# Kernel tuning notes

Hardware: AMD Instinct MI355X
Metric: run time of the kernel (lower is better)

Reference implementation:

```python
import jax, jax.numpy as jnp
import numpy as np

B, T, H, K = 2048, 200, 256, 8


def setup_inputs() -> dict:
    key = jax.random.key(0)
    ks = jax.random.split(key, 8)
    s = 1.0 / np.sqrt(H)  # torch nn.Linear default init range
    vm = jax.random.uniform(ks[5], (B, T)) < 0.6
    vm = vm.at[:, :3].set(True)  # guarantee >=3 valid visits so history_mask is non-empty
    return {
        "current_state": jax.random.normal(ks[0], (B, H), jnp.float32),
        "state_sequence": jax.random.normal(ks[1], (B, T, H), jnp.float32),
        "visit_mask": vm,
        "Wq": jax.random.uniform(ks[2], (H, H), jnp.float32, -s, s),
        "bq": jnp.zeros((H,), jnp.float32),
        "Wk": jax.random.uniform(ks[3], (H, H), jnp.float32, -s, s),
        "bk": jnp.zeros((H,), jnp.float32),
        "Wv": jax.random.uniform(ks[4], (H, H), jnp.float32, -s, s),
        "bv": jnp.zeros((H,), jnp.float32),
    }


def reference(current_state, state_sequence, visit_mask, Wq, bq, Wk, bk, Wv, bv):
    mask = visit_mask.astype(bool)
    valid_counts = mask.sum(axis=1)  # (B,)
    t_idx = jnp.arange(T)[None, :]
    # attend only to visits strictly before the last valid one
    history_mask = mask & (t_idx < (valid_counts - 1)[:, None])

    q = current_state @ Wq + bq                      # (B,H)
    k = state_sequence @ Wk + bk                     # (B,T,H)
    v = jax.nn.relu(state_sequence @ Wv + bv)        # dropout is identity in eval

    scores = jnp.einsum('bth,bh->bt', k, q) / np.sqrt(H).astype(np.float32)
    scores = jnp.where(history_mask, scores, -1e9)
    attn = jax.nn.softmax(scores, axis=-1)
    attn = jnp.where(history_mask, attn, 0.0)
    norm = attn.sum(-1, keepdims=True)
    attn = attn / jnp.where(norm > 0, norm, 1.0)

    # vectorized per-row top-K sparsify + renormalize (replaces the python loop)
    masked = jnp.where(history_mask, attn, -1.0)
    vals, idx = jax.lax.top_k(masked, K)             # (B,K)
    keep_vals = jnp.maximum(vals, 0.0)               # invalid slots had -1 -> contribute 0
    sparse = jnp.zeros_like(attn).at[jnp.arange(B)[:, None], idx].set(keep_vals)
    eps = jnp.finfo(attn.dtype).eps
    attn = sparse / jnp.maximum(sparse.sum(-1, keepdims=True), eps)

    summary = jnp.einsum('bth,bt->bh', v, attn)
    has_history = history_mask.any(axis=1, keepdims=True)
    summary = jnp.where(has_history, summary, 0.0)

    # selected visit indices (top-K of final weights, -1 where outside history)
    _, midx = jax.lax.top_k(jnp.where(history_mask, attn, -1.0), K)
    sel_mask = jnp.take_along_axis(history_mask, midx, axis=1)
    selected = jnp.where(sel_mask, midx, -1).astype(jnp.int32)

    return summary, attn, selected
```

## Files before the change

### kernel.cpp

```cpp
#include <hip/hip_runtime.h>
#include <cstddef>

#define BB 2048
#define TT 200
#define HH 256
#define KK 8
#define XP 260

#define WS_M2T 0
#define WS_D   65536
#define WS_E   65792
#define WS_F   66048
#define WS_IDX 66112
#define WS_W   82496

__global__ __launch_bounds__(256) void prep_kernel(
    const float* __restrict__ Wq, const float* __restrict__ bq,
    const float* __restrict__ Wk, const float* __restrict__ bk,
    float* __restrict__ M2T, float* __restrict__ dvec,
    float* __restrict__ evec, float* __restrict__ fsc) {
  const int l = blockIdx.x, i = threadIdx.x;
  __shared__ float s_wq[HH], s_bq[HH], s_bk[HH], s_red[HH];
  s_wq[i] = Wq[(size_t)l * HH + i];
  s_bq[i] = bq[i];
  s_bk[i] = bk[i];
  __syncthreads();
  const float* wk = Wk + (size_t)i * HH;
  float acc = 0.f, dd = 0.f;
#pragma unroll 8
  for (int j = 0; j < HH; ++j) {
    float wkj = wk[j];
    acc += s_wq[j] * wkj;
    dd  += s_bq[j] * wkj;
  }
  M2T[(size_t)l * HH + i] = acc;
  if (l == 0) dvec[i] = dd;
  s_red[i] = s_wq[i] * s_bk[i];
  __syncthreads();
  for (int s = 128; s > 0; s >>= 1) {
    if (i < s) s_red[i] += s_red[i + s];
    __syncthreads();
  }
  if (i == 0) {
    evec[l] = s_red[0];
    if (l == 0) {
      float ff = 0.f;
      for (int j = 0; j < HH; ++j) ff += s_bq[j] * s_bk[j];
      *fsc = ff;
    }
  }
}

__global__ __launch_bounds__(256) void attn_kernel(
    const float* __restrict__ CS, const float* __restrict__ X,
    const int* __restrict__ VM,
    const float* __restrict__ M2T, const float* __restrict__ dvec,
    const float* __restrict__ evec, const float* __restrict__ fsc,
    float* __restrict__ out, int* __restrict__ wsIdx, float* __restrict__ wsW) {
  const int tid = threadIdx.x, b = blockIdx.x;
  __shared__ float s_qk[HH], s_sc[TT], s_cand[TT], s_red[HH];
  __shared__ int   s_hist[TT];
  __shared__ int   s_cnt;
  __shared__ float s_qb, s_dS;
  __shared__ int   s_selI[KK];
  __shared__ float s_selV[KK];

  int m = 0;
  if (tid < TT) m = (VM[(size_t)b * TT + tid] != 0) ? 1 : 0;
  if (tid == 0) s_cnt = 0;
  __syncthreads();
  unsigned long long bal = __ballot(m);
  if ((tid & 63) == 0) atomicAdd(&s_cnt, (int)__popcll(bal));

  const float* csr = CS + (size_t)b * HH;
  float acc = dvec[tid];
#pragma unroll 4
  for (int l = 0; l < HH; ++l) acc += csr[l] * M2T[(size_t)l * HH + tid];
  s_qk[tid] = acc * 0.0625f;
  s_red[tid] = evec[tid] * csr[tid];
  __syncthreads();
  const int cnt = s_cnt;
  if (tid < TT) s_hist[tid] = (m && (tid < cnt - 1)) ? 1 : 0;
  for (int s = 128; s > 0; s >>= 1) {
    if (tid < s) s_red[tid] += s_red[tid + s];
    __syncthreads();
  }
  if (tid == 0) s_qb = (s_red[0] + fsc[0]) * 0.0625f;
  __syncthreads();

  {
    const int w = tid >> 6, lane = tid & 63;
    const float* xrow = X + (size_t)b * TT * HH;
    const float4 q4 = ((const float4*)s_qk)[lane];
    const float qb = s_qb;
#pragma unroll 2
    for (int t = w * 50; t < w * 50 + 50; ++t) {
      float4 xv = *(const float4*)(xrow + (size_t)t * HH + lane * 4);
      float p = xv.x * q4.x + xv.y * q4.y + xv.z * q4.z + xv.w * q4.w;
#pragma unroll
      for (int off = 32; off; off >>= 1) p += __shfl_xor(p, off);
      if (lane == 0) s_sc[t] = p + qb;
    }
  }
  __syncthreads();

  float v = (tid < TT && s_hist[tid]) ? s_sc[tid] : -3.4e38f;
  s_red[tid] = v;
  __syncthreads();
  for (int s = 128; s > 0; s >>= 1) {
    if (tid < s) s_red[tid] = fmaxf(s_red[tid], s_red[tid + s]);
    __syncthreads();
  }
  const float mx = s_red[0];
  __syncthreads();
  float p = (tid < TT && s_hist[tid]) ? expf(s_sc[tid] - mx) : 0.f;
  s_red[tid] = p;
  __syncthreads();
  for (int s = 128; s > 0; s >>= 1) {
    if (tid < s) s_red[tid] += s_red[tid + s];
    __syncthreads();
  }
  const float denom = s_red[0];
  __syncthreads();
  if (tid < TT) s_cand[tid] = s_hist[tid] ? (p / denom) : -1.0f;
  __syncthreads();

  if (tid < 64) {
    float lv[4]; int lt[4];
#pragma unroll
    for (int q = 0; q < 4; ++q) {
      int t = tid + 64 * q;
      lv[q] = (t < TT) ? s_cand[t] : -2.0f;
      lt[q] = t;
    }
    for (int r = 0; r < KK; ++r) {
      float bv = -2.5f; int bi = 1 << 30;
#pragma unroll
      for (int q = 0; q < 4; ++q)
        if (lv[q] > bv) { bv = lv[q]; bi = lt[q]; }
#pragma unroll
      for (int off = 32; off; off >>= 1) {
        float ov = __shfl_xor(bv, off);
        int   oi = __shfl_xor(bi, off);
        if (ov > bv || (ov == bv && oi < bi)) { bv = ov; bi = oi; }
      }
      if (tid == 0) { s_selI[r] = bi; s_selV[r] = bv; }
#pragma unroll
      for (int q = 0; q < 4; ++q)
        if (lt[q] == bi) lv[q] = -3.0f;
    }
    if (tid == 0) {
      float S = 0.f;
      for (int r = 0; r < KK; ++r) S += fmaxf(s_selV[r], 0.f);
      s_dS = fmaxf(S, 1.1920929e-07f);
    }
  }
  __syncthreads();

  float* out_attn = out + (size_t)BB * HH + (size_t)b * TT;
  if (tid < TT) out_attn[tid] = 0.f;
  __syncthreads();
  if (tid < KK) {
    float vvv = s_selV[tid];
    int   bi  = s_selI[tid];
    float wf  = fmaxf(vvv, 0.f) / s_dS;
    int ok = (vvv >= 0.f);
    if (ok) out_attn[bi] = wf;
    out[(size_t)BB * HH + (size_t)BB * TT + (size_t)b * KK + tid] =
        ok ? (float)bi : -1.0f;
    wsIdx[b * KK + tid] = ok ? bi : 0;
    wsW[b * KK + tid] = wf;
  }
}

__global__ __launch_bounds__(256) void summ_kernel(
    const float* __restrict__ X, const float* __restrict__ Wv,
    const float* __restrict__ bvv,
    const int* __restrict__ wsIdx, const float* __restrict__ wsW,
    float* __restrict__ out) {
  const int tid = threadIdx.x, bb = blockIdx.x;
  __shared__ float xs[64 * XP];
  __shared__ int   s_gi[64];
  __shared__ float s_w[64];
  if (tid < 64) {
    s_gi[tid] = wsIdx[bb * 64 + tid];
    s_w[tid]  = wsW[bb * 64 + tid];
  }
  __syncthreads();
#pragma unroll
  for (int it = 0; it < 16; ++it) {
    int fidx = it * 256 + tid;
    int row = fidx >> 6, c = fidx & 63;
    int bloc = bb * 8 + (row >> 3);
    int t = s_gi[row];
    float4 xv = *(const float4*)(X + ((size_t)bloc * TT + t) * HH + c * 4);
    *(float4*)(xs + row * XP + c * 4) = xv;
  }
  __syncthreads();

  const int ty = tid >> 5, tx = tid & 31;
  float accr[8][8];
#pragma unroll
  for (int r = 0; r < 8; ++r)
#pragma unroll
    for (int c = 0; c < 8; ++c) accr[r][c] = 0.f;

  const float* wvp = Wv + tx * 8;
  for (int ig = 0; ig < 64; ++ig) {
    float4 a4[8];
#pragma unroll
    for (int r = 0; r < 8; ++r)
      a4[r] = *(const float4*)(xs + (ty * 8 + r) * XP + ig * 4);
#pragma unroll
    for (int k = 0; k < 4; ++k) {
      const float* wrow = wvp + (size_t)(ig * 4 + k) * HH;
      float4 w0 = *(const float4*)(wrow);
      float4 w1 = *(const float4*)(wrow + 4);
#pragma unroll
      for (int r = 0; r < 8; ++r) {
        float av = (k == 0) ? a4[r].x : (k == 1) ? a4[r].y
                 : (k == 2) ? a4[r].z : a4[r].w;
        accr[r][0] += av * w0.x; accr[r][1] += av * w0.y;
        accr[r][2] += av * w0.z; accr[r][3] += av * w0.w;
        accr[r][4] += av * w1.x; accr[r][5] += av * w1.y;
        accr[r][6] += av * w1.z; accr[r][7] += av * w1.w;
      }
    }
  }
  float w8[8];
#pragma unroll
  for (int r = 0; r < 8; ++r) w8[r] = s_w[ty * 8 + r];
  float4 b0 = *(const float4*)(bvv + tx * 8);
  float4 b1 = *(const float4*)(bvv + tx * 8 + 4);
  float bc[8] = {b0.x, b0.y, b0.z, b0.w, b1.x, b1.y, b1.z, b1.w};
  float ob[8];
#pragma unroll
  for (int c = 0; c < 8; ++c) {
    float s = 0.f;
#pragma unroll
    for (int r = 0; r < 8; ++r) s += w8[r] * fmaxf(accr[r][c] + bc[c], 0.f);
    ob[c] = s;
  }
  float* op = out + (size_t)(bb * 8 + ty) * HH + tx * 8;
  *(float4*)(op)     = make_float4(ob[0], ob[1], ob[2], ob[3]);
  *(float4*)(op + 4) = make_float4(ob[4], ob[5], ob[6], ob[7]);
}

extern "C" void kernel_launch(void* const* d_in, const int* in_sizes, int n_in,
                              void* d_out, int out_size, void* d_ws, size_t ws_size,
                              hipStream_t stream) {
  const float* cs  = (const float*)d_in[0];
  const float* X   = (const float*)d_in[1];
  const int*   vm  = (const int*)d_in[2];
  const float* Wq  = (const float*)d_in[3];
  const float* bq  = (const float*)d_in[4];
  const float* Wk  = (const float*)d_in[5];
  const float* bk  = (const float*)d_in[6];
  const float* Wv  = (const float*)d_in[7];
  const float* bvp = (const float*)d_in[8];
  float* out = (float*)d_out;
  float* ws  = (float*)d_ws;

  float* M2T  = ws + WS_M2T;
  float* dvec = ws + WS_D;
  float* evec = ws + WS_E;
  float* fsc  = ws + WS_F;
  int*   wsI  = (int*)(ws + WS_IDX);
  float* wsW  = ws + WS_W;

  hipLaunchKernelGGL(prep_kernel, dim3(HH), dim3(HH), 0, stream,
                     Wq, bq, Wk, bk, M2T, dvec, evec, fsc);
  hipLaunchKernelGGL(attn_kernel, dim3(BB), dim3(HH), 0, stream,
                     cs, X, vm, M2T, dvec, evec, fsc, out, wsI, wsW);
  hipLaunchKernelGGL(summ_kernel, dim3(BB / 8), dim3(HH), 0, stream,
                     X, Wv, bvp, wsI, wsW, out);
}
```

Baseline: 656.0 us.

## Fuse value projection into attention kernel and restructure Q·Wk precompute

Rewrites the pipeline. The Wq·Wk product becomes a shared-memory tiled GEMM, the bias terms move to a separate reduction kernel, and the per-row q·M projection moves into a batched kernel that processes 8 rows per block. The value projection over the selected top-K rows is fused into the attention kernel, which removes the separate summary kernel and its workspace round trip. Block reductions now use wavefront shuffles instead of tree reductions over shared memory, and score loads are unrolled by 4. The trade-off is more launches and loss of Wv reuse across 64 rows in the fused GEMV.

New measurement: 741.7 us. 13.1% more time.

```diff
diff --git a/kernel.cpp b/kernel.cpp
--- a/kernel.cpp
+++ b/kernel.cpp
@@ -5,124 +5,206 @@
 #define TT 200
 #define HH 256
 #define KK 8
-#define XP 260
-
-#define WS_M2T 0
-#define WS_D   65536
-#define WS_E   65792
-#define WS_F   66048
-#define WS_IDX 66112
-#define WS_W   82496
-
-__global__ __launch_bounds__(256) void prep_kernel(
+
+#define WS_M2T  0
+#define WS_EVEC 65792
+#define WS_F    66048
+#define WS_QK   66304
+
+__device__ __forceinline__ float wred_sum(float v) {
+#pragma unroll
+  for (int off = 32; off; off >>= 1) v += __shfl_xor(v, off);
+  return v;
+}
+__device__ __forceinline__ float wred_max(float v) {
+#pragma unroll
+  for (int off = 32; off; off >>= 1) v = fmaxf(v, __shfl_xor(v, off));
+  return v;
+}
+
+__global__ __launch_bounds__(256) void prep_gemm(
+    const float* __restrict__ Wq, const float* __restrict__ Wk,
+    float* __restrict__ M2T) {
+  const int tid = threadIdx.x;
+  const int l0 = (blockIdx.x >> 2) * 64, i0 = (blockIdx.x & 3) * 64;
+  __shared__ float As[64][68], Bs[64][68];
+  const int tl = tid >> 4, ti = tid & 15;
+  float acc[4][4];
+#pragma unroll
+  for (int r = 0; r < 4; ++r)
+#pragma unroll
+    for (int c = 0; c < 4; ++c) acc[r][c] = 0.f;
+
+  for (int kc = 0; kc < 4; ++kc) {
+    const int k0 = kc * 64;
+#pragma unroll
+    for (int it = 0; it < 4; ++it) {
+      int idx = it * 256 + tid;
+      int row = idx >> 4, c4 = idx & 15;
+      *(float4*)(&As[row][c4 * 4]) =
+          *(const float4*)(Wq + (size_t)(l0 + row) * HH + k0 + c4 * 4);
+      *(float4*)(&Bs[row][c4 * 4]) =
+          *(const float4*)(Wk + (size_t)(i0 + row) * HH + k0 + c4 * 4);
+    }
+    __syncthreads();
+#pragma unroll 4
+    for (int k4 = 0; k4 < 16; ++k4) {
+      float4 a4[4], b4[4];
+#pragma unroll
+      for (int r = 0; r < 4; ++r) a4[r] = *(const float4*)(&As[tl * 4 + r][k4 * 4]);
+#pragma unroll
+      for (int c = 0; c < 4; ++c) b4[c] = *(const float4*)(&Bs[ti * 4 + c][k4 * 4]);
+#pragma unroll
+      for (int r = 0; r < 4; ++r)
+#pragma unroll
+        for (int c = 0; c < 4; ++c)
+          acc[r][c] += a4[r].x * b4[c].x + a4[r].y * b4[c].y +
+                       a4[r].z * b4[c].z + a4[r].w * b4[c].w;
+    }
+    __syncthreads();
+  }
+#pragma unroll
+  for (int r = 0; r < 4; ++r) {
+    float4 o = make_float4(acc[r][0], acc[r][1], acc[r][2], acc[r][3]);
+    *(float4*)(M2T + (size_t)(l0 + tl * 4 + r) * HH + i0 + ti * 4) = o;
+  }
+}
+
+__global__ __launch_bounds__(256) void bias_kernel(
     const float* __restrict__ Wq, const float* __restrict__ bq,
     const float* __restrict__ Wk, const float* __restrict__ bk,
-    float* __restrict__ M2T, float* __restrict__ dvec,
-    float* __restrict__ evec, float* __restrict__ fsc) {
-  const int l = blockIdx.x, i = threadIdx.x;
-  __shared__ float s_wq[HH], s_bq[HH], s_bk[HH], s_red[HH];
-  s_wq[i] = Wq[(size_t)l * HH + i];
-  s_bq[i] = bq[i];
-  s_bk[i] = bk[i];
-  __syncthreads();
-  const float* wk = Wk + (size_t)i * HH;
-  float acc = 0.f, dd = 0.f;
-#pragma unroll 8
-  for (int j = 0; j < HH; ++j) {
-    float wkj = wk[j];
-    acc += s_wq[j] * wkj;
-    dd  += s_bq[j] * wkj;
-  }
-  M2T[(size_t)l * HH + i] = acc;
-  if (l == 0) dvec[i] = dd;
-  s_red[i] = s_wq[i] * s_bk[i];
-  __syncthreads();
-  for (int s = 128; s > 0; s >>= 1) {
-    if (i < s) s_red[i] += s_red[i + s];
-    __syncthreads();
-  }
-  if (i == 0) {
-    evec[l] = s_red[0];
-    if (l == 0) {
-      float ff = 0.f;
-      for (int j = 0; j < HH; ++j) ff += s_bq[j] * s_bk[j];
-      *fsc = ff;
-    }
-  }
-}
-
-__global__ __launch_bounds__(256) void attn_kernel(
+    float* __restrict__ M2T, float* __restrict__ evec, float* __restrict__ fsc) {
+  const int id = blockIdx.x, tid = threadIdx.x;
+  __shared__ float s4[4];
+  const float* row;
+  const float* vec;
+  float* outp;
+  if (id < 256)      { row = Wk + (size_t)id * HH;        vec = bq; outp = M2T + (size_t)256 * HH + id; }
+  else if (id < 512) { row = Wq + (size_t)(id - 256) * HH; vec = bk; outp = evec + (id - 256); }
+  else               { row = bk;                           vec = bq; outp = fsc; }
+  float p = row[tid] * vec[tid];
+  p = wred_sum(p);
+  if ((tid & 63) == 0) s4[tid >> 6] = p;
+  __syncthreads();
+  if (tid == 0) *outp = s4[0] + s4[1] + s4[2] + s4[3];
+}
+
+__global__ __launch_bounds__(256, 4) void qkg_kernel(
+    const float* __restrict__ CS, const float* __restrict__ M2T,
+    float* __restrict__ QK) {
+  const int tid = threadIdx.x, bb = blockIdx.x;
+  __shared__ float s_cs[8][260];
+#pragma unroll
+  for (int it = 0; it < 2; ++it) {
+    int idx = it * 256 + tid;
+    int row = idx >> 6, c4 = idx & 63;
+    *(float4*)(&s_cs[row][c4 * 4]) =
+        *(const float4*)(CS + (size_t)(bb * 8 + row) * HH + c4 * 4);
+  }
+  if (tid < 8) s_cs[tid][256] = 1.0f;
+  __syncthreads();
+  const int bloc = tid >> 5, tx = tid & 31;
+  float acc[8];
+#pragma unroll
+  for (int c = 0; c < 8; ++c) acc[c] = 0.f;
+#pragma unroll 4
+  for (int l = 0; l < 257; ++l) {
+    float a = s_cs[bloc][l];
+    const float* mr = M2T + (size_t)l * HH + tx * 8;
+    float4 m0 = *(const float4*)(mr);
+    float4 m1 = *(const float4*)(mr + 4);
+    acc[0] += a * m0.x; acc[1] += a * m0.y; acc[2] += a * m0.z; acc[3] += a * m0.w;
+    acc[4] += a * m1.x; acc[5] += a * m1.y; acc[6] += a * m1.z; acc[7] += a * m1.w;
+  }
+  float* op = QK + (size_t)(bb * 8 + bloc) * HH + tx * 8;
+  *(float4*)(op)     = make_float4(acc[0] * 0.0625f, acc[1] * 0.0625f,
+                                   acc[2] * 0.0625f, acc[3] * 0.0625f);
+  *(float4*)(op + 4) = make_float4(acc[4] * 0.0625f, acc[5] * 0.0625f,
+                                   acc[6] * 0.0625f, acc[7] * 0.0625f);
+}
+
+__global__ __launch_bounds__(256, 4) void attn_kernel(
     const float* __restrict__ CS, const float* __restrict__ X,
     const int* __restrict__ VM,
-    const float* __restrict__ M2T, const float* __restrict__ dvec,
-    const float* __restrict__ evec, const float* __restrict__ fsc,
-    float* __restrict__ out, int* __restrict__ wsIdx, float* __restrict__ wsW) {
+    const float* __restrict__ QK, const float* __restrict__ evec,
+    const float* __restrict__ fsc,
+    const float* __restrict__ Wv, const float* __restrict__ bvv,
+    float* __restrict__ out) {
   const int tid = threadIdx.x, b = blockIdx.x;
-  __shared__ float s_qk[HH], s_sc[TT], s_cand[TT], s_red[HH];
+  const int w = tid >> 6, lane = tid & 63;
+  __shared__ float s_qk[HH];
+  __shared__ float s_sc[TT], s_cand[TT];
   __shared__ int   s_hist[TT];
-  __shared__ int   s_cnt;
-  __shared__ float s_qb, s_dS;
+  __shared__ float s_c4[4], s_r4[4], s_m4[4];
   __shared__ int   s_selI[KK];
   __shared__ float s_selV[KK];
-
-  int m = 0;
-  if (tid < TT) m = (VM[(size_t)b * TT + tid] != 0) ? 1 : 0;
-  if (tid == 0) s_cnt = 0;
-  __syncthreads();
+  __shared__ float s_dS;
+  __shared__ float xs[8][264];
+  __shared__ float red[4][260];
+
+  int m = (tid < TT) ? (VM[(size_t)b * TT + tid] != 0) : 0;
   unsigned long long bal = __ballot(m);
-  if ((tid & 63) == 0) atomicAdd(&s_cnt, (int)__popcll(bal));
-
-  const float* csr = CS + (size_t)b * HH;
-  float acc = dvec[tid];
-#pragma unroll 4
-  for (int l = 0; l < HH; ++l) acc += csr[l] * M2T[(size_t)l * HH + tid];
-  s_qk[tid] = acc * 0.0625f;
-  s_red[tid] = evec[tid] * csr[tid];
-  __syncthreads();
-  const int cnt = s_cnt;
+  if (lane == 0) s_c4[w] = (float)__popcll(bal);
+  s_qk[tid] = QK[(size_t)b * HH + tid];
+  float rq = CS[(size_t)b * HH + tid] * evec[tid];
+  rq = wred_sum(rq);
+  if (lane == 0) s_r4[w] = rq;
+  __syncthreads();
+
+  const int cnt = (int)(s_c4[0] + s_c4[1] + s_c4[2] + s_c4[3]);
   if (tid < TT) s_hist[tid] = (m && (tid < cnt - 1)) ? 1 : 0;
-  for (int s = 128; s > 0; s >>= 1) {
-    if (tid < s) s_red[tid] += s_red[tid + s];
-    __syncthreads();
-  }
-  if (tid == 0) s_qb = (s_red[0] + fsc[0]) * 0.0625f;
-  __syncthreads();
+  const float qb = (s_r4[0] + s_r4[1] + s_r4[2] + s_r4[3] + fsc[0]) * 0.0625f;
 
   {
-    const int w = tid >> 6, lane = tid & 63;
     const float* xrow = X + (size_t)b * TT * HH;
     const float4 q4 = ((const float4*)s_qk)[lane];
-    const float qb = s_qb;
-#pragma unroll 2
-    for (int t = w * 50; t < w * 50 + 50; ++t) {
+    const int tb = w * 50;
+    for (int i = 0; i < 48; i += 4) {
+      const float* p0 = xrow + (size_t)(tb + i) * HH + lane * 4;
+      float4 xa = *(const float4*)(p0);
+      float4 xb = *(const float4*)(p0 + HH);
+      float4 xc = *(const float4*)(p0 + 2 * HH);
+      float4 xd = *(const float4*)(p0 + 3 * HH);
+      float pa = xa.x * q4.x + xa.y * q4.y + xa.z * q4.z + xa.w * q4.w;
+      float pb = xb.x * q4.x + xb.y * q4.y + xb.z * q4.z + xb.w * q4.w;
+      float pc = xc.x * q4.x + xc.y * q4.y + xc.z * q4.z + xc.w * q4.w;
+      float pd = xd.x * q4.x + xd.y * q4.y + xd.z * q4.z + xd.w * q4.w;
+#pragma unroll
+      for (int off = 32; off; off >>= 1) {
+        pa += __shfl_xor(pa, off);
+        pb += __shfl_xor(pb, off);
+        pc += __shfl_xor(pc, off);
+        pd += __shfl_xor(pd, off);
+      }
+      if (lane == 0) {
+        s_sc[tb + i]     = pa + qb;
+        s_sc[tb + i + 1] = pb + qb;
+        s_sc[tb + i + 2] = pc + qb;
+        s_sc[tb + i + 3] = pd + qb;
+      }
+    }
+#pragma unroll
+    for (int t = tb + 48; t < tb + 50; ++t) {
       float4 xv = *(const float4*)(xrow + (size_t)t * HH + lane * 4);
       float p = xv.x * q4.x + xv.y * q4.y + xv.z * q4.z + xv.w * q4.w;
-#pragma unroll
-      for (int off = 32; off; off >>= 1) p += __shfl_xor(p, off);
+      p = wred_sum(p);
       if (lane == 0) s_sc[t] = p + qb;
     }
   }
   __syncthreads();
 
-  float v = (tid < TT && s_hist[tid]) ? s_sc[tid] : -3.4e38f;
-  s_red[tid] = v;
-  __syncthreads();
-  for (int s = 128; s > 0; s >>= 1) {
-    if (tid < s) s_red[tid] = fmaxf(s_red[tid], s_red[tid + s]);
-    __syncthreads();
-  }
-  const float mx = s_red[0];
-  __syncthreads();
-  float p = (tid < TT && s_hist[tid]) ? expf(s_sc[tid] - mx) : 0.f;
-  s_red[tid] = p;
-  __syncthreads();
-  for (int s = 128; s > 0; s >>= 1) {
-    if (tid < s) s_red[tid] += s_red[tid + s];
-    __syncthreads();
-  }
-  const float denom = s_red[0];
-  __syncthreads();
-  if (tid < TT) s_cand[tid] = s_hist[tid] ? (p / denom) : -1.0f;
+  const int hist = (tid < TT) ? s_hist[tid] : 0;
+  float v = hist ? s_sc[tid] : -3.4e38f;
+  float wm = wred_max(v);
+  if (lane == 0) s_m4[w] = wm;
+  __syncthreads();
+  const float mx = fmaxf(fmaxf(s_m4[0], s_m4[1]), fmaxf(s_m4[2], s_m4[3]));
+  float p = hist ? expf(v - mx) : 0.f;
+  float ws_ = wred_sum(p);
+  if (lane == 0) s_r4[w] = ws_;
+  __syncthreads();
+  const float denom = s_r4[0] + s_r4[1] + s_r4[2] + s_r4[3];
+  if (tid < TT) s_cand[tid] = hist ? (p / denom) : -1.0f;
   __syncthreads();
 
   if (tid < 64) {
@@ -151,11 +233,59 @@
     }
     if (tid == 0) {
       float S = 0.f;
+#pragma unroll
       for (int r = 0; r < KK; ++r) S += fmaxf(s_selV[r], 0.f);
       s_dS = fmaxf(S, 1.1920929e-07f);
     }
   }
   __syncthreads();
+
+  const int ty = tid >> 5, tx = tid & 31;
+  {
+    const int tsel = s_selI[ty];
+    const float* xr = X + ((size_t)b * TT + tsel) * HH + tx * 8;
+    *(float4*)(&xs[ty][tx * 8])     = *(const float4*)(xr);
+    *(float4*)(&xs[ty][tx * 8 + 4]) = *(const float4*)(xr + 4);
+  }
+  __syncthreads();
+  float acc[8];
+#pragma unroll
+  for (int c = 0; c < 8; ++c) acc[c] = 0.f;
+  {
+    const float* wvp = Wv + tx * 8;
+#pragma unroll 2
+    for (int k4 = 0; k4 < 64; ++k4) {
+      float4 a4 = *(const float4*)(&xs[ty][k4 * 4]);
+#pragma unroll
+      for (int kk = 0; kk < 4; ++kk) {
+        const float* wrow = wvp + (size_t)(k4 * 4 + kk) * HH;
+        float4 w0 = *(const float4*)(wrow);
+        float4 w1 = *(const float4*)(wrow + 4);
+        float av = (kk == 0) ? a4.x : (kk == 1) ? a4.y : (kk == 2) ? a4.z : a4.w;
+        acc[0] += av * w0.x; acc[1] += av * w0.y; acc[2] += av * w0.z; acc[3] += av * w0.w;
+        acc[4] += av * w1.x; acc[5] += av * w1.y; acc[6] += av * w1.z; acc[7] += av * w1.w;
+      }
+    }
+  }
+  {
+    const float wr = fmaxf(s_selV[ty], 0.f) / s_dS;
+    float4 b0 = *(const float4*)(bvv + tx * 8);
+    float4 b1 = *(const float4*)(bvv + tx * 8 + 4);
+    float val[8];
+    val[0] = wr * fmaxf(acc[0] + b0.x, 0.f); val[1] = wr * fmaxf(acc[1] + b0.y, 0.f);
+    val[2] = wr * fmaxf(acc[2] + b0.z, 0.f); val[3] = wr * fmaxf(acc[3] + b0.w, 0.f);
+    val[4] = wr * fmaxf(acc[4] + b1.x, 0.f); val[5] = wr * fmaxf(acc[5] + b1.y, 0.f);
+    val[6] = wr * fmaxf(acc[6] + b1.z, 0.f); val[7] = wr * fmaxf(acc[7] + b1.w, 0.f);
+#pragma unroll
+    for (int c = 0; c < 8; ++c) val[c] += __shfl_xor(val[c], 32);
+    if ((tid & 32) == 0) {
+      *(float4*)(&red[w][tx * 8])     = make_float4(val[0], val[1], val[2], val[3]);
+      *(float4*)(&red[w][tx * 8 + 4]) = make_float4(val[4], val[5], val[6], val[7]);
+    }
+  }
+  __syncthreads();
+  out[(size_t)b * HH + tid] =
+      red[0][tid] + red[1][tid] + red[2][tid] + red[3][tid];
 
   float* out_attn = out + (size_t)BB * HH + (size_t)b * TT;
   if (tid < TT) out_attn[tid] = 0.f;
@@ -168,82 +298,7 @@
     if (ok) out_attn[bi] = wf;
     out[(size_t)BB * HH + (size_t)BB * TT + (size_t)b * KK + tid] =
         ok ? (float)bi : -1.0f;
-    wsIdx[b * KK + tid] = ok ? bi : 0;
-    wsW[b * KK + tid] = wf;
-  }
-}
-
-__global__ __launch_bounds__(256) void summ_kernel(
-    const float* __restrict__ X, const float* __restrict__ Wv,
-    const float* __restrict__ bvv,
-    const int* __restrict__ wsIdx, const float* __restrict__ wsW,
-    float* __restrict__ out) {
-  const int tid = threadIdx.x, bb = blockIdx.x;
-  __shared__ float xs[64 * XP];
-  __shared__ int   s_gi[64];
-  __shared__ float s_w[64];
-  if (tid < 64) {
-    s_gi[tid] = wsIdx[bb * 64 + tid];
-    s_w[tid]  = wsW[bb * 64 + tid];
-  }
-  __syncthreads();
-#pragma unroll
-  for (int it = 0; it < 16; ++it) {
-    int fidx = it * 256 + tid;
-    int row = fidx >> 6, c = fidx & 63;
-    int bloc = bb * 8 + (row >> 3);
-    int t = s_gi[row];
-    float4 xv = *(const float4*)(X + ((size_t)bloc * TT + t) * HH + c * 4);
-    *(float4*)(xs + row * XP + c * 4) = xv;
-  }
-  __syncthreads();
-
-  const int ty = tid >> 5, tx = tid & 31;
-  float accr[8][8];
-#pragma unroll
-  for (int r = 0; r < 8; ++r)
-#pragma unroll
-    for (int c = 0; c < 8; ++c) accr[r][c] = 0.f;
-
-  const float* wvp = Wv + tx * 8;
-  for (int ig = 0; ig < 64; ++ig) {
-    float4 a4[8];
-#pragma unroll
-    for (int r = 0; r < 8; ++r)
-      a4[r] = *(const float4*)(xs + (ty * 8 + r) * XP + ig * 4);
-#pragma unroll
-    for (int k = 0; k < 4; ++k) {
-      const float* wrow = wvp + (size_t)(ig * 4 + k) * HH;
-      float4 w0 = *(const float4*)(wrow);
-      float4 w1 = *(const float4*)(wrow + 4);
-#pragma unroll
-      for (int r = 0; r < 8; ++r) {
-        float av = (k == 0) ? a4[r].x : (k == 1) ? a4[r].y
-                 : (k == 2) ? a4[r].z : a4[r].w;
-        accr[r][0] += av * w0.x; accr[r][1] += av * w0.y;
-        accr[r][2] += av * w0.z; accr[r][3] += av * w0.w;
-        accr[r][4] += av * w1.x; accr[r][5] += av * w1.y;
-        accr[r][6] += av * w1.z; accr[r][7] += av * w1.w;
-      }
-    }
-  }
-  float w8[8];
-#pragma unroll
-  for (int r = 0; r < 8; ++r) w8[r] = s_w[ty * 8 + r];
-  float4 b0 = *(const float4*)(bvv + tx * 8);
-  float4 b1 = *(const float4*)(bvv + tx * 8 + 4);
-  float bc[8] = {b0.x, b0.y, b0.z, b0.w, b1.x, b1.y, b1.z, b1.w};
-  float ob[8];
-#pragma unroll
-  for (int c = 0; c < 8; ++c) {
-    float s = 0.f;
-#pragma unroll
-    for (int r = 0; r < 8; ++r) s += w8[r] * fmaxf(accr[r][c] + bc[c], 0.f);
-    ob[c] = s;
-  }
-  float* op = out + (size_t)(bb * 8 + ty) * HH + tx * 8;
-  *(float4*)(op)     = make_float4(ob[0], ob[1], ob[2], ob[3]);
-  *(float4*)(op + 4) = make_float4(ob[4], ob[5], ob[6], ob[7]);
+  }
 }
 
 extern "C" void kernel_launch(void* const* d_in, const int* in_sizes, int n_in,
@@ -262,16 +317,15 @@
   float* ws  = (float*)d_ws;
 
   float* M2T  = ws + WS_M2T;
-  float* dvec = ws + WS_D;
-  float* evec = ws + WS_E;
+  float* evec = ws + WS_EVEC;
   float* fsc  = ws + WS_F;
-  int*   wsI  = (int*)(ws + WS_IDX);
-  float* wsW  = ws + WS_W;
-
-  hipLaunchKernelGGL(prep_kernel, dim3(HH), dim3(HH), 0, stream,
-                     Wq, bq, Wk, bk, M2T, dvec, evec, fsc);
-  hipLaunchKernelGGL(attn_kernel, dim3(BB), dim3(HH), 0, stream,
-                     cs, X, vm, M2T, dvec, evec, fsc, out, wsI, wsW);
-  hipLaunchKernelGGL(summ_kernel, dim3(BB / 8), dim3(HH), 0, stream,
-                     X, Wv, bvp, wsI, wsW, out);
-}
+  float* QK   = ws + WS_QK;
+
+  hipLaunchKernelGGL(prep_gemm, dim3(16), dim3(256), 0, stream, Wq, Wk, M2T);
+  hipLaunchKernelGGL(bias_kernel, dim3(513), dim3(256), 0, stream,
+                     Wq, bq, Wk, bk, M2T, evec, fsc);
+  hipLaunchKernelGGL(qkg_kernel, dim3(BB / 8), dim3(256), 0, stream,
+                     cs, M2T, QK);
+  hipLaunchKernelGGL(attn_kernel, dim3(BB), dim3(256), 0, stream,
+                     cs, X, vm, QK, evec, fsc, Wv, bvp, out);
+}
```
